# Kernel optimization log

Measured on AMD Instinct MI355X. Metric: run time of the kernel, lower is better.

## Reference

```python
import jax, jax.numpy as jnp
import numpy as np

B, S, D = 8, 1024, 1024
H = 16
HD = D // H
FFN = 4096
BN = 64  # adapter bottleneck
ADAPTER_SCALE = 0.1
EPS = 1e-5


def _ln(x, g, b):
    m = jnp.mean(x, axis=-1, keepdims=True)
    v = jnp.mean(jnp.square(x - m), axis=-1, keepdims=True)
    return (x - m) * jax.lax.rsqrt(v + EPS) * g + b


def setup_inputs() -> dict:
    key = jax.random.key(0)
    ks = jax.random.split(key, 16)
    sd = 0.02
    # weights stored [in, out] (math identical to torch's x @ W.T with W [out,in])
    return {
        "x": jax.random.normal(ks[0], (B, S, D), jnp.float32),
        "ln1_g": jnp.ones((D,), jnp.float32),
        "ln1_b": jnp.zeros((D,), jnp.float32),
        "wq": jax.random.normal(ks[1], (D, D), jnp.float32) * sd,
        "wk": jax.random.normal(ks[2], (D, D), jnp.float32) * sd,
        "wv": jax.random.normal(ks[3], (D, D), jnp.float32) * sd,
        "wo": jax.random.normal(ks[4], (D, D), jnp.float32) * sd,
        "bo": jnp.zeros((D,), jnp.float32),
        "ln2_g": jnp.ones((D,), jnp.float32),
        "ln2_b": jnp.zeros((D,), jnp.float32),
        "w1": jax.random.normal(ks[5], (D, FFN), jnp.float32) * sd,
        "b1": jnp.zeros((FFN,), jnp.float32),
        "w2": jax.random.normal(ks[6], (FFN, D), jnp.float32) * sd,
        "b2": jnp.zeros((D,), jnp.float32),
        "aln_g": jnp.ones((D,), jnp.float32),
        "aln_b": jnp.zeros((D,), jnp.float32),
        "wd": jax.random.normal(ks[7], (D, BN), jnp.float32) * sd,
        "bd": jnp.zeros((BN,), jnp.float32),
        "wu": jax.random.normal(ks[8], (BN, D), jnp.float32) * sd,
        "bu": jnp.zeros((D,), jnp.float32),
    }


def reference(x, ln1_g, ln1_b, wq, wk, wv, wo, bo, ln2_g, ln2_b,
              w1, b1, w2, b2, aln_g, aln_b, wd, bd, wu, bu):
    b, s, d = x.shape
    scale = HD ** -0.5

    # --- attention branch ---
    h = _ln(x, ln1_g, ln1_b)
    q = (h @ wq).reshape(b, s, H, HD)
    k = (h @ wk).reshape(b, s, H, HD)
    v = (h @ wv).reshape(b, s, H, HD)
    scores = jnp.einsum('bqhd,bkhd->bhqk', q, k) * scale  # [B,H,S,S]
    probs = jax.nn.softmax(scores, axis=-1)
    attn = jnp.einsum('bhqk,bkhd->bqhd', probs, v).reshape(b, s, d)
    x = x + (attn @ wo + bo)

    # --- parallel adapter (LN-in, down-relu-up, scaled, no residual) ---
    a = _ln(x, aln_g, aln_b)
    adapt_x = (jax.nn.relu(a @ wd + bd) @ wu + bu) * ADAPTER_SCALE

    # --- MLP branch ---
    residual = x
    h2 = _ln(x, ln2_g, ln2_b)
    h2 = jax.nn.gelu(h2 @ w1 + b1, approximate=False)
    h2 = h2 @ w2 + b2
    h2 = h2 + adapt_x
    return residual + h2
```

## Files before the change

kernel.cpp:

```cpp
#include <hip/hip_runtime.h>
#include <hip/hip_bf16.h>
#include <cstdint>
#include <cstddef>

#define DI __device__ __forceinline__

typedef __attribute__((ext_vector_type(8))) short v8s;
typedef __attribute__((ext_vector_type(4))) float v4f;

DI void gload_lds16(const unsigned short* g, unsigned short* l) {
  __builtin_amdgcn_global_load_lds(
      (const __attribute__((address_space(1))) unsigned int*)g,
      (__attribute__((address_space(3))) unsigned int*)l, 16, 0, 0);
}

DI float bf2f(unsigned short u) { return __uint_as_float(((unsigned int)u) << 16); }
DI unsigned short f2bf(float f) {
  unsigned int u = __float_as_uint(f);
  u += 0x7FFFu + ((u >> 16) & 1u);
  return (unsigned short)(u >> 16);
}
DI unsigned int pack2(float a, float b) {
  return (unsigned int)f2bf(a) | ((unsigned int)f2bf(b) << 16);
}

__global__ __launch_bounds__(256) void transpose_cvt_k(
    const float* __restrict__ in, unsigned short* __restrict__ out, int R, int C) {
  __shared__ unsigned short t[32][33];
  const int j0 = blockIdx.x * 32, i0 = blockIdx.y * 32;
  const int tx = threadIdx.x & 31, ty = threadIdx.x >> 5;
#pragma unroll
  for (int r = 0; r < 32; r += 8) t[ty + r][tx] = f2bf(in[(size_t)(i0 + ty + r) * C + j0 + tx]);
  __syncthreads();
#pragma unroll
  for (int r = 0; r < 32; r += 8) out[(size_t)(j0 + ty + r) * R + i0 + tx] = t[tx][ty + r];
}

__global__ __launch_bounds__(256) void vtrans_k(
    const unsigned short* __restrict__ v, unsigned short* __restrict__ vt) {
  __shared__ unsigned short t[32][33];
  const int bh = blockIdx.z, b = bh >> 4, h = bh & 15;
  const int s0 = blockIdx.x * 32, d0 = blockIdx.y * 32;
  const int tx = threadIdx.x & 31, ty = threadIdx.x >> 5;
  const unsigned short* src = v + ((size_t)(b * 1024 + s0)) * 1024 + h * 64 + d0;
#pragma unroll
  for (int r = 0; r < 32; r += 8) t[ty + r][tx] = src[(size_t)(ty + r) * 1024 + tx];
  __syncthreads();
  unsigned short* dst = vt + ((size_t)bh * 64 + d0) * 1024 + s0;
#pragma unroll
  for (int r = 0; r < 32; r += 8) dst[(size_t)(ty + r) * 1024 + tx] = t[tx][ty + r];
}

__global__ __launch_bounds__(256) void ln_k(
    const float* __restrict__ x, const float* __restrict__ g,
    const float* __restrict__ b, unsigned short* __restrict__ out) {
  const int row = blockIdx.x;
  const float4 v = ((const float4*)(x + (size_t)row * 1024))[threadIdx.x];
  float s = v.x + v.y + v.z + v.w;
  float ss = v.x * v.x + v.y * v.y + v.z * v.z + v.w * v.w;
#pragma unroll
  for (int o = 1; o < 64; o <<= 1) { s += __shfl_xor(s, o); ss += __shfl_xor(ss, o); }
  __shared__ float red[8];
  const int wid = threadIdx.x >> 6, lane = threadIdx.x & 63;
  if (!lane) { red[wid] = s; red[4 + wid] = ss; }
  __syncthreads();
  s = red[0] + red[1] + red[2] + red[3];
  ss = red[4] + red[5] + red[6] + red[7];
  const float mean = s * (1.f / 1024.f);
  const float var = ss * (1.f / 1024.f) - mean * mean;
  const float rs = rsqrtf(var + 1e-5f);
  const float4 gv = ((const float4*)g)[threadIdx.x];
  const float4 bv = ((const float4*)b)[threadIdx.x];
  ushort4 ov;
  ov.x = f2bf((v.x - mean) * rs * gv.x + bv.x);
  ov.y = f2bf((v.y - mean) * rs * gv.y + bv.y);
  ov.z = f2bf((v.z - mean) * rs * gv.z + bv.z);
  ov.w = f2bf((v.w - mean) * rs * gv.w + bv.w);
  ((ushort4*)(out + (size_t)row * 1024))[threadIdx.x] = ov;
}

enum { EPI_NONE = 0, EPI_BIAS_RES = 1, EPI_GELU = 2, EPI_RELU = 3, EPI_SCALE_BIAS = 4, EPI_FINAL = 5 };

template <int BN, int EPI, typename CT>
__global__ __launch_bounds__(256) void gemm_k(
    const unsigned short* __restrict__ A, const unsigned short* __restrict__ Bt,
    CT* __restrict__ C, const float* __restrict__ bias,
    const float* __restrict__ res, const float* __restrict__ extra,
    int M, int N, int K) {
  constexpr int BM = 128, BK = 32;
  constexpr int WN = (BN == 128) ? 2 : 1;
  constexpr int MR = (BN == 128) ? 4 : 2;
  constexpr int NR = 4;
  __shared__ unsigned short sA[BM * BK];
  __shared__ unsigned short sB[BN * BK];
  const int tid = threadIdx.x;
  const int lane = tid & 63, wid = tid >> 6;
  const int wm = wid / WN, wn = wid % WN;
  const int l15 = lane & 15, l4 = lane >> 4;
  const int row0 = blockIdx.x * BM, col0 = blockIdx.y * BN;
  v4f acc[MR][NR] = {};
  const int rowA = wm * MR * 16;
  const int rowB = wn * NR * 16;
  for (int k0 = 0; k0 < K; k0 += BK) {
#pragma unroll
    for (int r = 0; r < (BM * BK) / (256 * 8); ++r) {
      int e = (r * 256 + tid) * 8;
      gload_lds16(A + (size_t)(row0 + (e >> 5)) * K + k0 + (e & 31), ((unsigned short*)sA) + e);
    }
#pragma unroll
    for (int r = 0; r < (BN * BK) / (256 * 8); ++r) {
      int e = (r * 256 + tid) * 8;
      gload_lds16(Bt + (size_t)(col0 + (e >> 5)) * K + k0 + (e & 31), ((unsigned short*)sB) + e);
    }
    __syncthreads();
    v8s af[MR], bfr[NR];
#pragma unroll
    for (int m = 0; m < MR; ++m) af[m] = *(const v8s*)(sA + (rowA + m * 16 + l15) * BK + l4 * 8);
#pragma unroll
    for (int n = 0; n < NR; ++n) bfr[n] = *(const v8s*)(sB + (rowB + n * 16 + l15) * BK + l4 * 8);
#pragma unroll
    for (int m = 0; m < MR; ++m)
#pragma unroll
      for (int n = 0; n < NR; ++n)
        acc[m][n] = __builtin_amdgcn_mfma_f32_16x16x32_bf16(af[m], bfr[n], acc[m][n], 0, 0, 0);
    __syncthreads();
  }
#pragma unroll
  for (int m = 0; m < MR; ++m) {
#pragma unroll
    for (int n = 0; n < NR; ++n) {
      const int col = col0 + rowB + n * 16 + l15;
      float bv = 0.f;
      if (EPI != EPI_NONE) bv = bias[col];
#pragma unroll
      for (int j = 0; j < 4; ++j) {
        const int row = row0 + rowA + m * 16 + l4 * 4 + j;
        const size_t idx = (size_t)row * N + col;
        float v = acc[m][n][j];
        if (EPI == EPI_BIAS_RES) v += bv + res[idx];
        else if (EPI == EPI_GELU) { v += bv; v = 0.5f * v * (1.f + erff(v * 0.70710678118f)); }
        else if (EPI == EPI_RELU) { v += bv; v = fmaxf(v, 0.f); }
        else if (EPI == EPI_SCALE_BIAS) { v = (v + bv) * 0.1f; }
        else if (EPI == EPI_FINAL) { v += bv + res[idx] + extra[idx]; }
        if constexpr (sizeof(CT) == 2) C[idx] = f2bf(v); else C[idx] = v;
      }
    }
  }
}

__global__ __launch_bounds__(256) void attn_k(
    const unsigned short* __restrict__ Q, const unsigned short* __restrict__ Kc,
    const unsigned short* __restrict__ VT, unsigned short* __restrict__ O) {
  const int bh = blockIdx.y, b = bh >> 4, h = bh & 15;
  const int q0 = blockIdx.x * 64;
  const int tid = threadIdx.x, lane = tid & 63, wid = tid >> 6;
  const int l15 = lane & 15, l4 = lane >> 4;
  __shared__ unsigned short sQ[64 * 64];
  __shared__ unsigned short sK[32 * 64];
  __shared__ unsigned short sV[64 * 32];
  const unsigned short* Qb = Q + ((size_t)(b * 1024 + q0)) * 1024 + h * 64;
  const unsigned short* Kb = Kc + ((size_t)(b * 1024)) * 1024 + h * 64;
  const unsigned short* Vb = VT + (size_t)bh * 64 * 1024;
#pragma unroll
  for (int r = 0; r < 2; ++r) {
    int e = (r * 256 + tid) * 8, qr = e >> 6, gs = ((e >> 3) & 7) ^ (qr & 7);
    gload_lds16(Qb + (size_t)qr * 1024 + gs * 8, ((unsigned short*)sQ) + e);
  }
  float m_run = -3e38f, l_run = 0.f;
  v4f oacc[4] = {};
  const int qrow = wid * 16 + l15;
  for (int k0 = 0; k0 < 1024; k0 += 32) {
    { int e = tid * 8, kr = e >> 6, gs = ((e >> 3) & 7) ^ (kr & 7);
      gload_lds16(Kb + (size_t)(k0 + kr) * 1024 + gs * 8, ((unsigned short*)sK) + e); }
    { int e = tid * 8, dr = e >> 5, gs = ((e >> 3) & 3) ^ (dr & 3) ^ ((dr >> 2) & 3);
      gload_lds16(Vb + (size_t)dr * 1024 + k0 + gs * 8, ((unsigned short*)sV) + e); }
    __syncthreads();
    v4f sc0 = {}, sc1 = {};
#pragma unroll
    for (int dh = 0; dh < 2; ++dh) {
      const int ga0 = (l4 + 4 * dh) ^ (l15 & 7);
      v8s a0 = *(const v8s*)(sK + l15 * 64 + ga0 * 8);
      const int kr1 = 16 + l15;
      const int ga1 = (l4 + 4 * dh) ^ (kr1 & 7);
      v8s a1 = *(const v8s*)(sK + kr1 * 64 + ga1 * 8);
      const int gb = (l4 + 4 * dh) ^ (qrow & 7);
      v8s bq = *(const v8s*)(sQ + qrow * 64 + gb * 8);
      sc0 = __builtin_amdgcn_mfma_f32_16x16x32_bf16(a0, bq, sc0, 0, 0, 0);
      sc1 = __builtin_amdgcn_mfma_f32_16x16x32_bf16(a1, bq, sc1, 0, 0, 0);
    }
    float s8[8];
    float smax = -3e38f;
#pragma unroll
    for (int j = 0; j < 4; ++j) { s8[j] = sc0[j] * 0.125f; s8[4 + j] = sc1[j] * 0.125f; }
#pragma unroll
    for (int i = 0; i < 8; ++i) smax = fmaxf(smax, s8[i]);
    smax = fmaxf(smax, __shfl_xor(smax, 16));
    smax = fmaxf(smax, __shfl_xor(smax, 32));
    const float m_new = fmaxf(m_run, smax);
    const float fac = __expf(m_run - m_new);
    float tsum = 0.f;
#pragma unroll
    for (int i = 0; i < 8; ++i) { s8[i] = __expf(s8[i] - m_new); tsum += s8[i]; }
    tsum += __shfl_xor(tsum, 16);
    tsum += __shfl_xor(tsum, 32);
    l_run = l_run * fac + tsum;
    m_run = m_new;
#pragma unroll
    for (int nb = 0; nb < 4; ++nb) {
      oacc[nb][0] *= fac; oacc[nb][1] *= fac; oacc[nb][2] *= fac; oacc[nb][3] *= fac;
    }
    const unsigned int w0 = pack2(s8[0], s8[1]), w1 = pack2(s8[2], s8[3]);
    const unsigned int w2 = pack2(s8[4], s8[5]), w3 = pack2(s8[6], s8[7]);
    const int cse = l4 >> 1;
    const int src0 = l15 + 32 * (l4 & 1);
    const int src1 = src0 + 16;
    const unsigned int t00 = __shfl((int)w0, src0), t20 = __shfl((int)w2, src0);
    const unsigned int t10 = __shfl((int)w1, src0), t30 = __shfl((int)w3, src0);
    const unsigned int t01 = __shfl((int)w0, src1), t21 = __shfl((int)w2, src1);
    const unsigned int t11 = __shfl((int)w1, src1), t31 = __shfl((int)w3, src1);
    union { unsigned int u[4]; v8s v; } pb;
    pb.u[0] = cse ? t20 : t00; pb.u[1] = cse ? t30 : t10;
    pb.u[2] = cse ? t21 : t01; pb.u[3] = cse ? t31 : t11;
#pragma unroll
    for (int nb = 0; nb < 4; ++nb) {
      const int drow = nb * 16 + l15;
      const int gv = l4 ^ (drow & 3) ^ ((drow >> 2) & 3);
      v8s vf = *(const v8s*)(sV + drow * 32 + gv * 8);
      oacc[nb] = __builtin_amdgcn_mfma_f32_16x16x32_bf16(vf, pb.v, oacc[nb], 0, 0, 0);
    }
    __syncthreads();
  }
  const float inv = 1.f / l_run;
  unsigned short* Or = O + ((size_t)(b * 1024 + q0 + wid * 16 + l15)) * 1024 + h * 64;
#pragma unroll
  for (int nb = 0; nb < 4; ++nb) {
    ushort4 st;
    st.x = f2bf(oacc[nb][0] * inv); st.y = f2bf(oacc[nb][1] * inv);
    st.z = f2bf(oacc[nb][2] * inv); st.w = f2bf(oacc[nb][3] * inv);
    *(ushort4*)(Or + nb * 16 + l4 * 4) = st;
  }
}

extern "C" void kernel_launch(void* const* d_in, const int* in_sizes, int n_in,
                              void* d_out, int out_size, void* d_ws, size_t ws_size,
                              hipStream_t stream) {
  (void)in_sizes; (void)n_in; (void)out_size;
  const float* x    = (const float*)d_in[0];
  const float* ln1g = (const float*)d_in[1];
  const float* ln1b = (const float*)d_in[2];
  const float* wq   = (const float*)d_in[3];
  const float* wk   = (const float*)d_in[4];
  const float* wv   = (const float*)d_in[5];
  const float* wo   = (const float*)d_in[6];
  const float* bo   = (const float*)d_in[7];
  const float* ln2g = (const float*)d_in[8];
  const float* ln2b = (const float*)d_in[9];
  const float* w1   = (const float*)d_in[10];
  const float* b1   = (const float*)d_in[11];
  const float* w2   = (const float*)d_in[12];
  const float* b2   = (const float*)d_in[13];
  const float* alng = (const float*)d_in[14];
  const float* alnb = (const float*)d_in[15];
  const float* wd   = (const float*)d_in[16];
  const float* bd   = (const float*)d_in[17];
  const float* wu   = (const float*)d_in[18];
  const float* bu   = (const float*)d_in[19];
  float* out = (float*)d_out;

  char* W = (char*)d_ws;
  size_t off = 0;
  auto allocB = [&](size_t bytes) { void* p = W + off; off += (bytes + 255) & ~(size_t)255; return p; };
  const size_t T = 8192;
  unsigned short* wqt = (unsigned short*)allocB(1024 * 1024 * 2);
  unsigned short* wkt = (unsigned short*)allocB(1024 * 1024 * 2);
  unsigned short* wvt = (unsigned short*)allocB(1024 * 1024 * 2);
  unsigned short* wot = (unsigned short*)allocB(1024 * 1024 * 2);
  unsigned short* w1t = (unsigned short*)allocB((size_t)4096 * 1024 * 2);
  unsigned short* w2t = (unsigned short*)allocB((size_t)4096 * 1024 * 2);
  unsigned short* wdt = (unsigned short*)allocB(64 * 1024 * 2);
  unsigned short* wut = (unsigned short*)allocB(64 * 1024 * 2);
  unsigned short* H   = (unsigned short*)allocB(T * 1024 * 2);
  unsigned short* Qb  = (unsigned short*)allocB(T * 1024 * 2);
  unsigned short* Kb  = (unsigned short*)allocB(T * 1024 * 2);
  unsigned short* Vb  = (unsigned short*)allocB(T * 1024 * 2);
  unsigned short* VT  = (unsigned short*)allocB(T * 1024 * 2);
  float* X2           = (float*)allocB(T * 1024 * 4);
  unsigned short* MID = (unsigned short*)allocB(T * 4096 * 2);
  unsigned short* DWN = VT;
  float* ADP          = (float*)Qb;
  if (ws_size < off) return;

  dim3 blk(256);
  transpose_cvt_k<<<dim3(32, 32), blk, 0, stream>>>(wq, wqt, 1024, 1024);
  transpose_cvt_k<<<dim3(32, 32), blk, 0, stream>>>(wk, wkt, 1024, 1024);
  transpose_cvt_k<<<dim3(32, 32), blk, 0, stream>>>(wv, wvt, 1024, 1024);
  transpose_cvt_k<<<dim3(32, 32), blk, 0, stream>>>(wo, wot, 1024, 1024);
  transpose_cvt_k<<<dim3(128, 32), blk, 0, stream>>>(w1, w1t, 1024, 4096);
  transpose_cvt_k<<<dim3(32, 128), blk, 0, stream>>>(w2, w2t, 4096, 1024);
  transpose_cvt_k<<<dim3(2, 32), blk, 0, stream>>>(wd, wdt, 1024, 64);
  transpose_cvt_k<<<dim3(32, 2), blk, 0, stream>>>(wu, wut, 64, 1024);

  ln_k<<<8192, blk, 0, stream>>>(x, ln1g, ln1b, H);
  gemm_k<128, EPI_NONE, unsigned short><<<dim3(64, 8), blk, 0, stream>>>(H, wqt, Qb, nullptr, nullptr, nullptr, 8192, 1024, 1024);
  gemm_k<128, EPI_NONE, unsigned short><<<dim3(64, 8), blk, 0, stream>>>(H, wkt, Kb, nullptr, nullptr, nullptr, 8192, 1024, 1024);
  gemm_k<128, EPI_NONE, unsigned short><<<dim3(64, 8), blk, 0, stream>>>(H, wvt, Vb, nullptr, nullptr, nullptr, 8192, 1024, 1024);
  vtrans_k<<<dim3(32, 2, 128), blk, 0, stream>>>(Vb, VT);
  attn_k<<<dim3(16, 128), blk, 0, stream>>>(Qb, Kb, VT, Vb);
  gemm_k<128, EPI_BIAS_RES, float><<<dim3(64, 8), blk, 0, stream>>>(Vb, wot, X2, bo, x, nullptr, 8192, 1024, 1024);
  ln_k<<<8192, blk, 0, stream>>>(X2, alng, alnb, H);
  gemm_k<64, EPI_RELU, unsigned short><<<dim3(64, 1), blk, 0, stream>>>(H, wdt, DWN, bd, nullptr, nullptr, 8192, 64, 1024);
  gemm_k<128, EPI_SCALE_BIAS, float><<<dim3(64, 8), blk, 0, stream>>>(DWN, wut, ADP, bu, nullptr, nullptr, 8192, 1024, 64);
  ln_k<<<8192, blk, 0, stream>>>(X2, ln2g, ln2b, H);
  gemm_k<128, EPI_GELU, unsigned short><<<dim3(64, 32), blk, 0, stream>>>(H, w1t, MID, b1, nullptr, nullptr, 8192, 4096, 1024);
  gemm_k<128, EPI_FINAL, float><<<dim3(64, 8), blk, 0, stream>>>(MID, w2t, out, b2, X2, ADP, 8192, 1024, 4096);
}
```

Before: 661.3 us.

## Add pipelined 8-wave GEMM with larger tiles and fuse QKV projections

Introduces a new 512-thread GEMM kernel with 128x256 or 256x256 tiles, BK=64, double-buffered LDS prefetch via direct global-to-LDS loads, XOR-swizzled LDS, wave priority hints and a workgroup index swizzle. It is used for the QKV, output-projection and both MLP GEMMs. The three Q/K/V weights are concatenated so a single GEMM produces a strided QKV buffer, and attention and the V-transpose now take a leading-dimension argument. The aim is to raise MFMA utilisation and hide global-load latency. The cost is higher register and LDS pressure and fewer blocks resident per CU.

After: 613.4 us. 7.2% less time.

```diff
diff --git a/kernel.cpp b/kernel.cpp
--- a/kernel.cpp
+++ b/kernel.cpp
@@ -37,14 +37,14 @@
 }
 
 __global__ __launch_bounds__(256) void vtrans_k(
-    const unsigned short* __restrict__ v, unsigned short* __restrict__ vt) {
+    const unsigned short* __restrict__ v, unsigned short* __restrict__ vt, int ld) {
   __shared__ unsigned short t[32][33];
   const int bh = blockIdx.z, b = bh >> 4, h = bh & 15;
   const int s0 = blockIdx.x * 32, d0 = blockIdx.y * 32;
   const int tx = threadIdx.x & 31, ty = threadIdx.x >> 5;
-  const unsigned short* src = v + ((size_t)(b * 1024 + s0)) * 1024 + h * 64 + d0;
-#pragma unroll
-  for (int r = 0; r < 32; r += 8) t[ty + r][tx] = src[(size_t)(ty + r) * 1024 + tx];
+  const unsigned short* src = v + (size_t)(b * 1024 + s0) * ld + h * 64 + d0;
+#pragma unroll
+  for (int r = 0; r < 32; r += 8) t[ty + r][tx] = src[(size_t)(ty + r) * ld + tx];
   __syncthreads();
   unsigned short* dst = vt + ((size_t)bh * 64 + d0) * 1024 + s0;
 #pragma unroll
@@ -80,6 +80,118 @@
 }
 
 enum { EPI_NONE = 0, EPI_BIAS_RES = 1, EPI_GELU = 2, EPI_RELU = 3, EPI_SCALE_BIAS = 4, EPI_FINAL = 5 };
+
+template <int BM, int BN, int EPI, typename CT>
+__global__ __launch_bounds__(512, 2) void gemm8_k(
+    const unsigned short* __restrict__ A, const unsigned short* __restrict__ Bt,
+    CT* __restrict__ C, const float* __restrict__ bias,
+    const float* __restrict__ res, const float* __restrict__ extra,
+    int M, int N, int K, int gm, int gn) {
+  constexpr int MF = BM / 32, NF = BN / 64, MPP = MF / 4;
+  constexpr int LA = BM / 64, LB = BN / 64, LT = LA + LB;
+  constexpr int BUFE = (BM + BN) * 64;
+  __shared__ unsigned short lds[BUFE * 2];
+  const int tid = threadIdx.x;
+  const int lane = tid & 63, wid = tid >> 6;
+  const int wm = wid >> 2, wn = wid & 3;
+  const int l15 = lane & 15, l4 = lane >> 4;
+  const int nwg = gm * gn;
+  const int bid = blockIdx.x;
+  const int swz = (bid % 8) * (nwg / 8) + bid / 8;
+  const int row0 = (swz / gn) * BM, col0 = (swz % gn) * BN;
+  const int NT = K >> 6;
+
+  const int srow = tid >> 3, sgr = tid & 7;
+  auto stA = [&](int kt, int b, int a) {
+    const unsigned short* s = A + (size_t)(row0 + a * 64 + srow) * K + kt * 64 + ((sgr ^ (srow & 7)) << 3);
+    gload_lds16(s, lds + b * BUFE + a * 4096 + tid * 8);
+  };
+  auto stB = [&](int kt, int b, int a) {
+    const unsigned short* s = Bt + (size_t)(col0 + a * 64 + srow) * K + kt * 64 + ((sgr ^ (srow & 7)) << 3);
+    gload_lds16(s, lds + b * BUFE + BM * 64 + a * 4096 + tid * 8);
+  };
+
+#pragma unroll
+  for (int e = 0; e < LA; ++e) stA(0, 0, e);
+#pragma unroll
+  for (int e = 0; e < LB; ++e) stB(0, 0, e);
+#pragma unroll
+  for (int e = 0; e < LB; ++e) stB(1, 1, e);
+  asm volatile("s_waitcnt vmcnt(%0)" ::"n"(LB) : "memory");
+  __builtin_amdgcn_s_barrier();
+
+  v4f acc[MF][NF] = {};
+  v8s bfr[NF][2];
+  for (int t = 0; t < NT; ++t) {
+    const int buf = t & 1;
+    const unsigned short* La = lds + buf * BUFE;
+    const unsigned short* Lb = lds + buf * BUFE + BM * 64;
+#pragma unroll
+    for (int p = 0; p < 4; ++p) {
+      if (p == 0) {
+#pragma unroll
+        for (int nf = 0; nf < NF; ++nf) {
+          const int r = wn * (BN / 4) + nf * 16 + l15;
+#pragma unroll
+          for (int kk = 0; kk < 2; ++kk)
+            bfr[nf][kk] = *(const v8s*)(Lb + r * 64 + ((kk * 32 + l4 * 8) ^ ((r & 7) << 3)));
+        }
+      }
+      v8s af[MPP][2];
+#pragma unroll
+      for (int mm = 0; mm < MPP; ++mm) {
+        const int r = wm * (BM / 2) + (p * MPP + mm) * 16 + l15;
+#pragma unroll
+        for (int kk = 0; kk < 2; ++kk)
+          af[mm][kk] = *(const v8s*)(La + r * 64 + ((kk * 32 + l4 * 8) ^ ((r & 7) << 3)));
+      }
+#pragma unroll
+      for (int e = p * LT / 4; e < (p + 1) * LT / 4; ++e) {
+        if (e < LA) { if (t + 1 < NT) stA(t + 1, buf ^ 1, e); }
+        else        { if (t + 2 < NT) stB(t + 2, buf, e - LA); }
+      }
+      __builtin_amdgcn_s_barrier();
+      asm volatile("s_waitcnt lgkmcnt(0)" ::: "memory");
+      __builtin_amdgcn_s_setprio(1);
+#pragma unroll
+      for (int mm = 0; mm < MPP; ++mm)
+#pragma unroll
+        for (int nf = 0; nf < NF; ++nf)
+#pragma unroll
+          for (int kk = 0; kk < 2; ++kk)
+            acc[p * MPP + mm][nf] = __builtin_amdgcn_mfma_f32_16x16x32_bf16(
+                af[mm][kk], bfr[nf][kk], acc[p * MPP + mm][nf], 0, 0, 0);
+      __builtin_amdgcn_s_setprio(0);
+      if (p == 3 && t + 1 < NT) {
+        if (t + 2 < NT) asm volatile("s_waitcnt vmcnt(%0)" ::"n"(LB) : "memory");
+        else            asm volatile("s_waitcnt vmcnt(0)" ::: "memory");
+      }
+      __builtin_amdgcn_s_barrier();
+    }
+  }
+
+#pragma unroll
+  for (int mf = 0; mf < MF; ++mf) {
+#pragma unroll
+    for (int nf = 0; nf < NF; ++nf) {
+      const int col = col0 + wn * (BN / 4) + nf * 16 + l15;
+      float bv = 0.f;
+      if (EPI != EPI_NONE) bv = bias[col];
+#pragma unroll
+      for (int j = 0; j < 4; ++j) {
+        const int row = row0 + wm * (BM / 2) + mf * 16 + l4 * 4 + j;
+        const size_t idx = (size_t)row * N + col;
+        float v = acc[mf][nf][j];
+        if (EPI == EPI_BIAS_RES) v += bv + res[idx];
+        else if (EPI == EPI_GELU) { v += bv; v = 0.5f * v * (1.f + erff(v * 0.70710678118f)); }
+        else if (EPI == EPI_RELU) { v += bv; v = fmaxf(v, 0.f); }
+        else if (EPI == EPI_SCALE_BIAS) { v = (v + bv) * 0.1f; }
+        else if (EPI == EPI_FINAL) { v += bv + res[idx] + extra[idx]; }
+        if constexpr (sizeof(CT) == 2) C[idx] = f2bf(v); else C[idx] = v;
+      }
+    }
+  }
+}
 
 template <int BN, int EPI, typename CT>
 __global__ __launch_bounds__(256) void gemm_k(
@@ -113,16 +225,16 @@
       gload_lds16(Bt + (size_t)(col0 + (e >> 5)) * K + k0 + (e & 31), ((unsigned short*)sB) + e);
     }
     __syncthreads();
-    v8s af[MR], bfr[NR];
+    v8s af[MR], bfr2[NR];
 #pragma unroll
     for (int m = 0; m < MR; ++m) af[m] = *(const v8s*)(sA + (rowA + m * 16 + l15) * BK + l4 * 8);
 #pragma unroll
-    for (int n = 0; n < NR; ++n) bfr[n] = *(const v8s*)(sB + (rowB + n * 16 + l15) * BK + l4 * 8);
+    for (int n = 0; n < NR; ++n) bfr2[n] = *(const v8s*)(sB + (rowB + n * 16 + l15) * BK + l4 * 8);
 #pragma unroll
     for (int m = 0; m < MR; ++m)
 #pragma unroll
       for (int n = 0; n < NR; ++n)
-        acc[m][n] = __builtin_amdgcn_mfma_f32_16x16x32_bf16(af[m], bfr[n], acc[m][n], 0, 0, 0);
+        acc[m][n] = __builtin_amdgcn_mfma_f32_16x16x32_bf16(af[m], bfr2[n], acc[m][n], 0, 0, 0);
     __syncthreads();
   }
 #pragma unroll
@@ -150,7 +262,7 @@
 
 __global__ __launch_bounds__(256) void attn_k(
     const unsigned short* __restrict__ Q, const unsigned short* __restrict__ Kc,
-    const unsigned short* __restrict__ VT, unsigned short* __restrict__ O) {
+    const unsigned short* __restrict__ VT, unsigned short* __restrict__ O, int ldqk) {
   const int bh = blockIdx.y, b = bh >> 4, h = bh & 15;
   const int q0 = blockIdx.x * 64;
   const int tid = threadIdx.x, lane = tid & 63, wid = tid >> 6;
@@ -158,20 +270,20 @@
   __shared__ unsigned short sQ[64 * 64];
   __shared__ unsigned short sK[32 * 64];
   __shared__ unsigned short sV[64 * 32];
-  const unsigned short* Qb = Q + ((size_t)(b * 1024 + q0)) * 1024 + h * 64;
-  const unsigned short* Kb = Kc + ((size_t)(b * 1024)) * 1024 + h * 64;
+  const unsigned short* Qb = Q + (size_t)(b * 1024 + q0) * ldqk + h * 64;
+  const unsigned short* Kb = Kc + (size_t)(b * 1024) * ldqk + h * 64;
   const unsigned short* Vb = VT + (size_t)bh * 64 * 1024;
 #pragma unroll
   for (int r = 0; r < 2; ++r) {
     int e = (r * 256 + tid) * 8, qr = e >> 6, gs = ((e >> 3) & 7) ^ (qr & 7);
-    gload_lds16(Qb + (size_t)qr * 1024 + gs * 8, ((unsigned short*)sQ) + e);
+    gload_lds16(Qb + (size_t)qr * ldqk + gs * 8, ((unsigned short*)sQ) + e);
   }
   float m_run = -3e38f, l_run = 0.f;
   v4f oacc[4] = {};
   const int qrow = wid * 16 + l15;
   for (int k0 = 0; k0 < 1024; k0 += 32) {
     { int e = tid * 8, kr = e >> 6, gs = ((e >> 3) & 7) ^ (kr & 7);
-      gload_lds16(Kb + (size_t)(k0 + kr) * 1024 + gs * 8, ((unsigned short*)sK) + e); }
+      gload_lds16(Kb + (size_t)(k0 + kr) * ldqk + gs * 8, ((unsigned short*)sK) + e); }
     { int e = tid * 8, dr = e >> 5, gs = ((e >> 3) & 3) ^ (dr & 3) ^ ((dr >> 2) & 3);
       gload_lds16(Vb + (size_t)dr * 1024 + k0 + gs * 8, ((unsigned short*)sV) + e); }
     __syncthreads();
@@ -231,7 +343,7 @@
     __syncthreads();
   }
   const float inv = 1.f / l_run;
-  unsigned short* Or = O + ((size_t)(b * 1024 + q0 + wid * 16 + l15)) * 1024 + h * 64;
+  unsigned short* Or = O + (size_t)(b * 1024 + q0 + wid * 16 + l15) * 1024 + h * 64;
 #pragma unroll
   for (int nb = 0; nb < 4; ++nb) {
     ushort4 st;
@@ -271,29 +383,26 @@
   size_t off = 0;
   auto allocB = [&](size_t bytes) { void* p = W + off; off += (bytes + 255) & ~(size_t)255; return p; };
   const size_t T = 8192;
-  unsigned short* wqt = (unsigned short*)allocB(1024 * 1024 * 2);
-  unsigned short* wkt = (unsigned short*)allocB(1024 * 1024 * 2);
-  unsigned short* wvt = (unsigned short*)allocB(1024 * 1024 * 2);
-  unsigned short* wot = (unsigned short*)allocB(1024 * 1024 * 2);
-  unsigned short* w1t = (unsigned short*)allocB((size_t)4096 * 1024 * 2);
-  unsigned short* w2t = (unsigned short*)allocB((size_t)4096 * 1024 * 2);
-  unsigned short* wdt = (unsigned short*)allocB(64 * 1024 * 2);
-  unsigned short* wut = (unsigned short*)allocB(64 * 1024 * 2);
-  unsigned short* H   = (unsigned short*)allocB(T * 1024 * 2);
-  unsigned short* Qb  = (unsigned short*)allocB(T * 1024 * 2);
-  unsigned short* Kb  = (unsigned short*)allocB(T * 1024 * 2);
-  unsigned short* Vb  = (unsigned short*)allocB(T * 1024 * 2);
-  unsigned short* VT  = (unsigned short*)allocB(T * 1024 * 2);
-  float* X2           = (float*)allocB(T * 1024 * 4);
-  unsigned short* MID = (unsigned short*)allocB(T * 4096 * 2);
+  unsigned short* wqkvt = (unsigned short*)allocB((size_t)3072 * 1024 * 2);
+  unsigned short* wot   = (unsigned short*)allocB((size_t)1024 * 1024 * 2);
+  unsigned short* w1t   = (unsigned short*)allocB((size_t)4096 * 1024 * 2);
+  unsigned short* w2t   = (unsigned short*)allocB((size_t)4096 * 1024 * 2);
+  unsigned short* wdt   = (unsigned short*)allocB(64 * 1024 * 2);
+  unsigned short* wut   = (unsigned short*)allocB(64 * 1024 * 2);
+  unsigned short* H     = (unsigned short*)allocB(T * 1024 * 2);
+  unsigned short* QKV   = (unsigned short*)allocB(T * 3072 * 2);
+  unsigned short* VT    = (unsigned short*)allocB(T * 1024 * 2);
+  float* X2             = (float*)allocB(T * 1024 * 4);
+  unsigned short* MID   = (unsigned short*)allocB(T * 4096 * 2);
+  unsigned short* AO  = MID;
   unsigned short* DWN = VT;
-  float* ADP          = (float*)Qb;
+  float* ADP          = (float*)QKV;
   if (ws_size < off) return;
 
   dim3 blk(256);
-  transpose_cvt_k<<<dim3(32, 32), blk, 0, stream>>>(wq, wqt, 1024, 1024);
-  transpose_cvt_k<<<dim3(32, 32), blk, 0, stream>>>(wk, wkt, 1024, 1024);
-  transpose_cvt_k<<<dim3(32, 32), blk, 0, stream>>>(wv, wvt, 1024, 1024);
+  transpose_cvt_k<<<dim3(32, 32), blk, 0, stream>>>(wq, wqkvt, 1024, 1024);
+  transpose_cvt_k<<<dim3(32, 32), blk, 0, stream>>>(wk, wqkvt + (size_t)1024 * 1024, 1024, 1024);
+  transpose_cvt_k<<<dim3(32, 32), blk, 0, stream>>>(wv, wqkvt + (size_t)2048 * 1024, 1024, 1024);
   transpose_cvt_k<<<dim3(32, 32), blk, 0, stream>>>(wo, wot, 1024, 1024);
   transpose_cvt_k<<<dim3(128, 32), blk, 0, stream>>>(w1, w1t, 1024, 4096);
   transpose_cvt_k<<<dim3(32, 128), blk, 0, stream>>>(w2, w2t, 4096, 1024);
@@ -301,16 +410,20 @@
   transpose_cvt_k<<<dim3(32, 2), blk, 0, stream>>>(wu, wut, 64, 1024);
 
   ln_k<<<8192, blk, 0, stream>>>(x, ln1g, ln1b, H);
-  gemm_k<128, EPI_NONE, unsigned short><<<dim3(64, 8), blk, 0, stream>>>(H, wqt, Qb, nullptr, nullptr, nullptr, 8192, 1024, 1024);
-  gemm_k<128, EPI_NONE, unsigned short><<<dim3(64, 8), blk, 0, stream>>>(H, wkt, Kb, nullptr, nullptr, nullptr, 8192, 1024, 1024);
-  gemm_k<128, EPI_NONE, unsigned short><<<dim3(64, 8), blk, 0, stream>>>(H, wvt, Vb, nullptr, nullptr, nullptr, 8192, 1024, 1024);
-  vtrans_k<<<dim3(32, 2, 128), blk, 0, stream>>>(Vb, VT);
-  attn_k<<<dim3(16, 128), blk, 0, stream>>>(Qb, Kb, VT, Vb);
-  gemm_k<128, EPI_BIAS_RES, float><<<dim3(64, 8), blk, 0, stream>>>(Vb, wot, X2, bo, x, nullptr, 8192, 1024, 1024);
+  gemm8_k<128, 256, EPI_NONE, unsigned short><<<768, 512, 0, stream>>>(
+      H, wqkvt, QKV, nullptr, nullptr, nullptr, 8192, 3072, 1024, 64, 12);
+  vtrans_k<<<dim3(32, 2, 128), blk, 0, stream>>>(QKV + 2048, VT, 3072);
+  attn_k<<<dim3(16, 128), blk, 0, stream>>>(QKV, QKV + 1024, VT, AO, 3072);
+  gemm8_k<128, 256, EPI_BIAS_RES, float><<<256, 512, 0, stream>>>(
+      AO, wot, X2, bo, x, nullptr, 8192, 1024, 1024, 64, 4);
   ln_k<<<8192, blk, 0, stream>>>(X2, alng, alnb, H);
-  gemm_k<64, EPI_RELU, unsigned short><<<dim3(64, 1), blk, 0, stream>>>(H, wdt, DWN, bd, nullptr, nullptr, 8192, 64, 1024);
-  gemm_k<128, EPI_SCALE_BIAS, float><<<dim3(64, 8), blk, 0, stream>>>(DWN, wut, ADP, bu, nullptr, nullptr, 8192, 1024, 64);
+  gemm_k<64, EPI_RELU, unsigned short><<<dim3(64, 1), blk, 0, stream>>>(
+      H, wdt, DWN, bd, nullptr, nullptr, 8192, 64, 1024);
+  gemm_k<128, EPI_SCALE_BIAS, float><<<dim3(64, 8), blk, 0, stream>>>(
+      DWN, wut, ADP, bu, nullptr, nullptr, 8192, 1024, 64);
   ln_k<<<8192, blk, 0, stream>>>(X2, ln2g, ln2b, H);
-  gemm_k<128, EPI_GELU, unsigned short><<<dim3(64, 32), blk, 0, stream>>>(H, w1t, MID, b1, nullptr, nullptr, 8192, 4096, 1024);
-  gemm_k<128, EPI_FINAL, float><<<dim3(64, 8), blk, 0, stream>>>(MID, w2t, out, b2, X2, ADP, 8192, 1024, 4096);
-}
+  gemm8_k<256, 256, EPI_GELU, unsigned short><<<512, 512, 0, stream>>>(
+      H, w1t, MID, b1, nullptr, nullptr, 8192, 4096, 1024, 32, 16);
+  gemm8_k<128, 256, EPI_FINAL, float><<<256, 512, 0, stream>>>(
+      MID, w2t, out, b2, X2, ADP, 8192, 1024, 4096, 64, 4);
+}
```
